# Optimization experiments

Measured on AMD Instinct MI355X. Metric: run time of the kernel, lower is better.

## Reference

```python
import jax, jax.numpy as jnp
import numpy as np

B, S, H = 1, 2048, 2048
NH, NKV, HD = 32, 8, 64
GROUPS = NH // NKV
KV_DIM = NKV * HD
COMP = int(S * 0.5)
FF = 5632  # round_up(2048*4*2/3, 256), fla GatedMLP convention
DEPTH = 2
EPS = 1e-6


def rmsnorm(x, w):
    var = jnp.mean(jnp.square(x), axis=-1, keepdims=True)
    return x * jax.lax.rsqrt(var + EPS) * w


def setup_inputs() -> dict:
    key = jax.random.key(0)
    ks = jax.random.split(key, 10)
    sc = 0.02
    return {
        "hidden_states": jax.random.normal(ks[0], (B, S, H), jnp.float32),
        "comp_w": jax.random.normal(ks[1], (COMP, S), jnp.float32) * sc,
        "comp_b": jnp.zeros((COMP,), jnp.float32),
        "q_w": jax.random.normal(ks[2], (H, H), jnp.float32) * sc,
        "k_w": jax.random.normal(ks[3], (KV_DIM, H), jnp.float32) * sc,
        "v_w": jax.random.normal(ks[4], (KV_DIM, H), jnp.float32) * sc,
        "o_w": jax.random.normal(ks[5], (H, H), jnp.float32) * sc,
        "attn_norm_w": jnp.ones((H,), jnp.float32),
        "mlp_norm_w": jnp.ones((H,), jnp.float32),
        "gate_w": jax.random.normal(ks[6], (FF, H), jnp.float32) * sc,
        "up_w": jax.random.normal(ks[7], (FF, H), jnp.float32) * sc,
        "down_w": jax.random.normal(ks[8], (H, FF), jnp.float32) * sc,
    }


def reference(hidden_states, comp_w, comp_b, q_w, k_w, v_w, o_w,
              attn_norm_w, mlp_norm_w, gate_w, up_w, down_w):
    # init_compressed_tokens: Linear over the sequence axis
    # (b,s,h) -> transpose -> (b,h,s) @ W^T -> (b,h,c) -> transpose -> (b,c,h)
    compressed = jnp.einsum('bsh,cs->bch', hidden_states, comp_w) + comp_b[None, :, None]

    for _ in range(DEPTH):
        residual = jnp.concatenate([hidden_states, compressed], axis=1)  # (b, s+c, h)
        ct = rmsnorm(compressed, attn_norm_w)
        q = (ct @ q_w.T).reshape(B, COMP, NH, HD)
        k = (residual @ k_w.T).reshape(B, S + COMP, NKV, HD)
        v = (residual @ v_w.T).reshape(B, S + COMP, NKV, HD)
        # GQA expand (repeat_interleave along head dim)
        k = jnp.repeat(k, GROUPS, axis=2)
        v = jnp.repeat(v, GROUPS, axis=2)
        scores = jnp.einsum('bsnk,btnk->bsnt', q, k) / (HD ** 0.5)
        attn = jax.nn.softmax(scores, axis=-1)
        o = jnp.einsum('bsnt,btnk->bsnk', attn, v).reshape(B, COMP, H)
        compressed = o @ o_w.T + ct
        ct2 = rmsnorm(compressed, mlp_norm_w)
        mlp_out = (jax.nn.silu(ct2 @ gate_w.T) * (ct2 @ up_w.T)) @ down_w.T
        compressed = mlp_out + ct2
    return compressed
```

## Files before the change

### kernel.cpp

```cpp
#include <hip/hip_runtime.h>
#include <math.h>

constexpr int S_   = 2048;
constexpr int H_   = 2048;
constexpr int NH_  = 32;
constexpr int NKV_ = 8;
constexpr int HD_  = 64;
constexpr int GROUPS_ = NH_ / NKV_;
constexpr int KV_  = NKV_ * HD_;
constexpr int KV2_ = 2 * KV_;
constexpr int COMP_ = 1024;
constexpr int FF_  = 5632;
constexpr int GU2_ = 2 * FF_;
constexpr int TOT_ = S_ + COMP_;
constexpr float EPS_ = 1e-6f;
constexpr int SK_ = 4;
constexpr int SP_ = 2;
constexpr float LOG2E_ = 1.44269504088896340736f;

typedef __attribute__((ext_vector_type(4))) float f32x4;
typedef __attribute__((ext_vector_type(8))) short bf16x8;
typedef __attribute__((ext_vector_type(8))) ushort u16x8;

__device__ __forceinline__ ushort f2bf(float x) {
    union { float f; unsigned u; } v; v.f = x;
    unsigned r = v.u + 0x7fffu + ((v.u >> 16) & 1u);
    return (ushort)(r >> 16);
}
__device__ __forceinline__ float bf2f(ushort x) {
    union { unsigned u; float f; } v; v.u = ((unsigned)x) << 16;
    return v.f;
}
__device__ __forceinline__ uint cvtpk_bf16(float lo, float hi) {
    uint r;
    asm("v_cvt_pk_bf16_f32 %0, %1, %2" : "=v"(r) : "v"(lo), "v"(hi));
    return r;
}

__global__ __launch_bounds__(256) void f2b_k(
    const float* __restrict__ x, ushort* __restrict__ y, int n4)
{
    int i = blockIdx.x * 256 + threadIdx.x;
    const int stride = gridDim.x * 256;
    for (; i < n4; i += stride) {
        float4 v = ((const float4*)x)[i];
        ushort4 r = {f2bf(v.x), f2bf(v.y), f2bf(v.z), f2bf(v.w)};
        ((ushort4*)y)[i] = r;
    }
}

__global__ __launch_bounds__(256) void f2b_gu(
    const float* __restrict__ gate, const float* __restrict__ up,
    ushort* __restrict__ dst, int n4)
{
    constexpr int H4 = H_ / 4;
    int i = blockIdx.x * 256 + threadIdx.x;
    const int stride = gridDim.x * 256;
    for (; i < n4; i += stride) {
        const int j = i / H4, c4 = i - j * H4;
        const float* src = ((j >> 4) & 1) ? up : gate;
        const int srow = ((j >> 5) << 4) | (j & 15);
        const float4 v = ((const float4*)src)[srow * H4 + c4];
        ushort4 r = {f2bf(v.x), f2bf(v.y), f2bf(v.z), f2bf(v.w)};
        ((ushort4*)dst)[i] = r;
    }
}

__global__ __launch_bounds__(256) void tpose64(
    const ushort* __restrict__ in, ushort* __restrict__ out,
    int R, int C, int ldi)
{
    __shared__ ushort T[64][72];
    const int r0 = blockIdx.x * 64, c0 = blockIdx.y * 64;
    const int row = threadIdx.x >> 2, seg = threadIdx.x & 3;

    const ushort* g = &in[(size_t)(r0 + row) * ldi + c0 + seg * 16];
    *(u16x8*)&T[row][seg * 16]     = *(const u16x8*)g;
    *(u16x8*)&T[row][seg * 16 + 8] = *(const u16x8*)(g + 8);
    __syncthreads();

    ushort tmp[16];
#pragma unroll
    for (int j = 0; j < 16; j++) tmp[j] = T[seg * 16 + j][row];
    ushort* go = &out[(size_t)(c0 + row) * R + r0 + seg * 16];
    *(u16x8*)go       = *(const u16x8*)&tmp[0];
    *(u16x8*)(go + 8) = *(const u16x8*)&tmp[8];
}

#define BARS do { __builtin_amdgcn_s_barrier(); __builtin_amdgcn_sched_barrier(0); } while (0)
#define VMW(n) asm volatile("s_waitcnt vmcnt(" #n ")" ::: "memory")
#define STG(gp, lp) __builtin_amdgcn_global_load_lds( \
    (const __attribute__((address_space(1))) void*)(gp), \
    (__attribute__((address_space(3))) void*)(lp), 16, 0, 0)
#define STA(bufA, R0, kt) STG(Ag + (size_t)(R0) * K + (kt) * 64, &(bufA)[((R0) + w * 8) * 64])
#define STB(bufB, R0, kt) STG(Bg + (size_t)(R0) * K + (kt) * 64, &(bufB)[((R0) + w * 8) * 64])

__device__ __forceinline__ void ldaq(bf16x8 (&aa)[2][2], const ushort* bufA,
                                     int m0, int aoff, int s0, int s1)
{
#pragma unroll
    for (int m = 0; m < 2; m++) {
        aa[m][0] = *(const bf16x8*)&bufA[aoff + (m0 + m) * 1024 + s0];
        aa[m][1] = *(const bf16x8*)&bufA[aoff + (m0 + m) * 1024 + s1];
    }
}
__device__ __forceinline__ void ldbq(bf16x8 (&bb)[4][2], const ushort* bufB,
                                     int boff, int s0, int s1)
{
#pragma unroll
    for (int nt = 0; nt < 4; nt++) {
        bb[nt][0] = *(const bf16x8*)&bufB[boff + nt * 1024 + s0];
        bb[nt][1] = *(const bf16x8*)&bufB[boff + nt * 1024 + s1];
    }
}
template <int M0>
__device__ __forceinline__ void mfmaq(f32x4 (&acc)[8][4], bf16x8 (&aa)[2][2],
                                      bf16x8 (&bb)[4][2])
{
    __builtin_amdgcn_s_setprio(1);
#pragma unroll
    for (int m = 0; m < 2; m++)
#pragma unroll
        for (int nt = 0; nt < 4; nt++) {
            acc[M0 + m][nt] = __builtin_amdgcn_mfma_f32_16x16x32_bf16(
                aa[m][0], bb[nt][0], acc[M0 + m][nt], 0, 0, 0);
            acc[M0 + m][nt] = __builtin_amdgcn_mfma_f32_16x16x32_bf16(
                aa[m][1], bb[nt][1], acc[M0 + m][nt], 0, 0, 0);
        }
    __builtin_amdgcn_s_setprio(0);
}

__global__ __launch_bounds__(512, 2) void gemm8ph(
    const ushort* __restrict__ A, const ushort* __restrict__ B,
    ushort* __restrict__ g, int N, int K)
{
    alignas(16) __shared__ ushort lds[4][16384];
    ushort* const lA0 = lds[0];
    ushort* const lB0 = lds[1];
    ushort* const lA1 = lds[2];
    ushort* const lB1 = lds[3];

    const int tid = threadIdx.x;
    const int w = tid >> 6, lane = tid & 63;
    const int wr = w >> 2, wc = w & 3;
    const int fr = lane & 15, fq = lane >> 4;
    const int xk = fr & 7;

    const int nwg = gridDim.x;
    const int nbn = N >> 8;
    int id = (int)blockIdx.x;
    if (!(nwg & 7)) id = (id & 7) * (nwg >> 3) + (id >> 3);
    const int bm = id / nbn, bn = id - bm * nbn;

    const int srow = lane >> 3;
    const int scol = ((lane & 7) ^ srow) << 3;
    const ushort* Ag = A + (size_t)(bm * 256 + w * 8 + srow) * K + scol;
    const ushort* Bg = B + (size_t)(bn * 256 + w * 8 + srow) * K + scol;

    const int aoff = (wr * 128 + fr) * 64;
    const int boff = (wc * 64 + fr) * 64;
    const int s0 = ((0 + fq) ^ xk) << 3;
    const int s1 = ((4 + fq) ^ xk) << 3;

    f32x4 acc[8][4];
#pragma unroll
    for (int i = 0; i < 8; i++)
#pragma unroll
        for (int j = 0; j < 4; j++) acc[i][j] = (f32x4){0.f, 0.f, 0.f, 0.f};

    bf16x8 aa[2][2], bb[4][2];

    STB(lB0, 0, 0);   STB(lB0, 64, 0);
    STA(lA0, 0, 0);   STA(lA0, 128, 0);
    STB(lB0, 128, 0); STB(lB0, 192, 0);
    STA(lA0, 64, 0);  STA(lA0, 192, 0);
    STB(lB1, 0, 1);   STB(lB1, 64, 1);
    STA(lA1, 0, 1);   STA(lA1, 128, 1);
    STB(lB1, 128, 1); STB(lB1, 192, 1);
    VMW(6);
    BARS;

    const int NITER = K >> 7;
    for (int i = 0; i < NITER - 1; i++) {
        const int t1 = 2 * i + 1, t2 = 2 * i + 2, t3 = 2 * i + 3;
        ldbq(bb, lB0, boff, s0, s1);
        ldaq(aa, lA0, 0, aoff, s0, s1);
        STA(lA1, 64, t1); STA(lA1, 192, t1);
        BARS; mfmaq<0>(acc, aa, bb); BARS;
        ldaq(aa, lA0, 2, aoff, s0, s1);
        STB(lB0, 0, t2); STB(lB0, 64, t2);
        BARS; mfmaq<2>(acc, aa, bb); BARS;
        ldaq(aa, lA0, 4, aoff, s0, s1);
        STA(lA0, 0, t2); STA(lA0, 128, t2);
        BARS; mfmaq<4>(acc, aa, bb); BARS;
        ldaq(aa, lA0, 6, aoff, s0, s1);
        STB(lB0, 128, t2); STB(lB0, 192, t2);
        BARS; mfmaq<6>(acc, aa, bb); VMW(6); BARS;
        ldbq(bb, lB1, boff, s0, s1);
        ldaq(aa, lA1, 0, aoff, s0, s1);
        STA(lA0, 64, t2); STA(lA0, 192, t2);
        BARS; mfmaq<0>(acc, aa, bb); BARS;
        ldaq(aa, lA1, 2, aoff, s0, s1);
        STB(lB1, 0, t3); STB(lB1, 64, t3);
        BARS; mfmaq<2>(acc, aa, bb); BARS;
        ldaq(aa, lA1, 4, aoff, s0, s1);
        STA(lA1, 0, t3); STA(lA1, 128, t3);
        BARS; mfmaq<4>(acc, aa, bb); BARS;
        ldaq(aa, lA1, 6, aoff, s0, s1);
        STB(lB1, 128, t3); STB(lB1, 192, t3);
        BARS; mfmaq<6>(acc, aa, bb); VMW(6); BARS;
    }
    {
        const int t1 = 2 * NITER - 1;
        ldbq(bb, lB0, boff, s0, s1);
        ldaq(aa, lA0, 0, aoff, s0, s1);
        STA(lA1, 64, t1); STA(lA1, 192, t1);
        BARS; mfmaq<0>(acc, aa, bb); BARS;
        ldaq(aa, lA0, 2, aoff, s0, s1);
        BARS; mfmaq<2>(acc, aa, bb); BARS;
        ldaq(aa, lA0, 4, aoff, s0, s1);
        BARS; mfmaq<4>(acc, aa, bb); BARS;
        ldaq(aa, lA0, 6, aoff, s0, s1);
        BARS; mfmaq<6>(acc, aa, bb); VMW(0); BARS;
        ldbq(bb, lB1, boff, s0, s1);
        ldaq(aa, lA1, 0, aoff, s0, s1);
        BARS; mfmaq<0>(acc, aa, bb); BARS;
        ldaq(aa, lA1, 2, aoff, s0, s1);
        BARS; mfmaq<2>(acc, aa, bb); BARS;
        ldaq(aa, lA1, 4, aoff, s0, s1);
        BARS; mfmaq<4>(acc, aa, bb); BARS;
        ldaq(aa, lA1, 6, aoff, s0, s1);
        mfmaq<6>(acc, aa, bb);
    }

    const int FFo = N >> 1;
#pragma unroll
    for (int mt = 0; mt < 8; mt++) {
#pragma unroll
        for (int u = 0; u < 2; u++) {
            const int col = (bn * 8 + wc * 2 + u) * 16 + fr;
#pragma unroll
            for (int r = 0; r < 4; r++) {
                const int row = bm * 256 + wr * 128 + mt * 16 + fq * 4 + r;
                const float xg = acc[mt][2 * u][r];
                const float xu = acc[mt][2 * u + 1][r];
                const float yv = xg / (1.f + __expf(-xg)) * xu;
                g[(size_t)row * FFo + col] = f2bf(yv);
            }
        }
    }
}

__global__ __launch_bounds__(256) void mfma_gemm_sk(
    const ushort* __restrict__ A, const ushort* __restrict__ B,
    float* __restrict__ part, int M, int N, int K, int Kc)
{
    __shared__ ushort Alds[128 * 32];
    __shared__ ushort Blds[128 * 32];

    const int tid  = threadIdx.x;
    const int w    = tid >> 6;
    const int lane = tid & 63;
    const int bm = blockIdx.y, bn = blockIdx.x, z = blockIdx.z;
    const int wr = w >> 1, wc = w & 1;
    const int fr = lane & 15;
    const int fq = lane >> 4;
    const int srow = lane >> 2;
    const int skof = (lane & 3) * 8;

    f32x4 acc[4][4];
#pragma unroll
    for (int i = 0; i < 4; i++)
#pragma unroll
        for (int j = 0; j < 4; j++)
            acc[i][j] = (f32x4){0.f, 0.f, 0.f, 0.f};

    const int kbeg = z * Kc;
    for (int k0 = kbeg; k0 < kbeg + Kc; k0 += 32) {
        __syncthreads();
#pragma unroll
        for (int i = 0; i < 2; i++) {
            const int slot = w * 2 + i;
            const ushort* ga = &A[(size_t)(bm * 128 + slot * 16 + srow) * K + k0 + skof];
            __builtin_amdgcn_global_load_lds(
                (const __attribute__((address_space(1))) void*)ga,
                (__attribute__((address_space(3))) void*)&Alds[slot * 512], 16, 0, 0);
            const ushort* gb = &B[(size_t)(bn * 128 + slot * 16 + srow) * K + k0 + skof];
            __builtin_amdgcn_global_load_lds(
                (const __attribute__((address_space(1))) void*)gb,
                (__attribute__((address_space(3))) void*)&Blds[slot * 512], 16, 0, 0);
        }
        __syncthreads();

        bf16x8 a[4], b[4];
#pragma unroll
        for (int mt = 0; mt < 4; mt++)
            a[mt] = *(const bf16x8*)&Alds[(wr * 64 + mt * 16 + fr) * 32 + fq * 8];
#pragma unroll
        for (int nt = 0; nt < 4; nt++)
            b[nt] = *(const bf16x8*)&Blds[(wc * 64 + nt * 16 + fr) * 32 + fq * 8];

#pragma unroll
        for (int mt = 0; mt < 4; mt++)
#pragma unroll
            for (int nt = 0; nt < 4; nt++)
                acc[mt][nt] = __builtin_amdgcn_mfma_f32_16x16x32_bf16(
                    a[mt], b[nt], acc[mt][nt], 0, 0, 0);
    }

    float* pz = part + (size_t)z * M * N;
#pragma unroll
    for (int mt = 0; mt < 4; mt++)
#pragma unroll
        for (int nt = 0; nt < 4; nt++)
#pragma unroll
            for (int r = 0; r < 4; r++) {
                const int row = bm * 128 + wr * 64 + mt * 16 + fq * 4 + r;
                const int col = bn * 128 + wc * 64 + nt * 16 + fr;
                pz[(size_t)row * N + col] = acc[mt][nt][r];
            }
}

__global__ __launch_bounds__(256) void sk_reduce(
    const float* __restrict__ part, int mn4, int n4,
    const float* __restrict__ bias, const float* __restrict__ addp,
    float oscale, float* __restrict__ outf, ushort* __restrict__ outb)
{
    const size_t mn = (size_t)mn4 * 4;
    int i = blockIdx.x * 256 + threadIdx.x;
    const int stride = gridDim.x * 256;
    for (; i < mn4; i += stride) {
        float4 v = ((const float4*)part)[i];
#pragma unroll
        for (int z = 1; z < SK_; z++) {
            const float4 pz = ((const float4*)(part + z * mn))[i];
            v.x += pz.x; v.y += pz.y; v.z += pz.z; v.w += pz.w;
        }
        v.x *= oscale; v.y *= oscale; v.z *= oscale; v.w *= oscale;
        if (bias) {
            const float bb = bias[i / n4];
            v.x += bb; v.y += bb; v.z += bb; v.w += bb;
        }
        if (addp) {
            const float4 ad = ((const float4*)addp)[i];
            v.x += ad.x; v.y += ad.y; v.z += ad.z; v.w += ad.w;
        }
        if (outf) ((float4*)outf)[i] = v;
        if (outb) {
            ushort4 r = {f2bf(v.x), f2bf(v.y), f2bf(v.z), f2bf(v.w)};
            ((ushort4*)outb)[i] = r;
        }
    }
}

__global__ __launch_bounds__(256) void sk_reduce_rms(
    const float* __restrict__ part, const float* __restrict__ bias,
    const float* __restrict__ addp, const float* __restrict__ w,
    ushort* __restrict__ residb, float* __restrict__ y,
    ushort* __restrict__ yb)
{
    constexpr size_t MN = (size_t)COMP_ * H_;
    const int row = blockIdx.x;
    const int t = threadIdx.x;
    __shared__ float red[256];

    float4 v[2];
#pragma unroll
    for (int j = 0; j < 2; j++) {
        const int c4 = t + j * 256;
        v[j] = ((const float4*)(part + (size_t)row * H_))[c4];
#pragma unroll
        for (int z = 1; z < SK_; z++) {
            const float4 pz = ((const float4*)(part + z * MN + (size_t)row * H_))[c4];
            v[j].x += pz.x; v[j].y += pz.y; v[j].z += pz.z; v[j].w += pz.w;
        }
        if (bias) {
            const float bb = bias[row];
            v[j].x += bb; v[j].y += bb; v[j].z += bb; v[j].w += bb;
        }
        if (addp) {
            const float4 ad = ((const float4*)(addp + (size_t)row * H_))[c4];
            v[j].x += ad.x; v[j].y += ad.y; v[j].z += ad.z; v[j].w += ad.w;
        }
        if (residb) {
            ushort4 r = {f2bf(v[j].x), f2bf(v[j].y), f2bf(v[j].z), f2bf(v[j].w)};
            ((ushort4*)(residb + (size_t)row * H_))[c4] = r;
        }
    }
    float s = 0.f;
#pragma unroll
    for (int j = 0; j < 2; j++)
        s += v[j].x * v[j].x + v[j].y * v[j].y + v[j].z * v[j].z + v[j].w * v[j].w;
    red[t] = s;
    __syncthreads();
    for (int k = 128; k > 0; k >>= 1) {
        if (t < k) red[t] += red[t + k];
        __syncthreads();
    }
    const float scale = rsqrtf(red[0] * (1.0f / H_) + EPS_);
#pragma unroll
    for (int j = 0; j < 2; j++) {
        const int c4 = t + j * 256;
        const float4 wv = ((const float4*)w)[c4];
        float4 nv;
        nv.x = v[j].x * scale * wv.x;
        nv.y = v[j].y * scale * wv.y;
        nv.z = v[j].z * scale * wv.z;
        nv.w = v[j].w * scale * wv.w;
        ((float4*)(y + (size_t)row * H_))[c4] = nv;
        ushort4 r = {f2bf(nv.x), f2bf(nv.y), f2bf(nv.z), f2bf(nv.w)};
        ((ushort4*)(yb + (size_t)row * H_))[c4] = r;
    }
}

__global__ __launch_bounds__(256) void attn_mfma(
    const ushort* __restrict__ q, const ushort* __restrict__ k, int ldk,
    const ushort* __restrict__ vt, float* __restrict__ attp,
    float* __restrict__ ml)
{
    constexpr int KSPAN = TOT_ / SP_;
    alignas(16) __shared__ ushort Kb[2][8 * 512];
    alignas(16) __shared__ ushort Vb[2][8 * 512];
    alignas(16) __shared__ ushort Ps[64 * 64];

    const int qt = blockIdx.x, h = blockIdx.y, z = blockIdx.z;
    const int kvh = h / GROUPS_;
    const int tid = threadIdx.x;
    const int w = tid >> 6, lane = tid & 63;
    const int fr = lane & 15, fq = lane >> 4;
    const int q0 = qt * 64;

    const ushort* qrow = &q[(size_t)(q0 + w * 16 + fr) * H_ + h * HD_];
    const bf16x8 bq0 = *(const bf16x8*)(qrow + fq * 8);
    const bf16x8 bq1 = *(const bf16x8*)(qrow + 32 + fq * 8);

    float m = -1e30f, l = 0.f;
    f32x4 acc[4];
#pragma unroll
    for (int nt = 0; nt < 4; nt++) acc[nt] = (f32x4){0.f, 0.f, 0.f, 0.f};

    const int t_beg = z * KSPAN;
    const ushort* kp = &k[(size_t)(t_beg + w * 16 + fr) * ldk + kvh * HD_ + fq * 8];
    const ushort* vp = &vt[(size_t)(kvh * HD_ + w * 16 + fr) * TOT_ + t_beg + fq * 8];

#define ASTG(gp, lp) __builtin_amdgcn_global_load_lds( \
    (const __attribute__((address_space(1))) void*)(gp), \
    (__attribute__((address_space(3))) void*)(lp), 16, 0, 0)

    ASTG(kp,      &Kb[0][w * 512]);
    ASTG(kp + 32, &Kb[0][(4 + w) * 512]);
    ASTG(vp,      &Vb[0][w * 512]);
    ASTG(vp + 32, &Vb[0][(4 + w) * 512]);
    asm volatile("s_waitcnt vmcnt(0)" ::: "memory");
    __syncthreads();
    const ushort* kn = kp + (size_t)64 * ldk;
    const ushort* vn = vp + 64;

    const int pxor = (fr & 7) << 4;
    char* const psb = (char*)&Ps[(w * 16 + fr) * 64];

    const int NT = KSPAN / 64;
    int cur = 0;
    for (int t = 0; t < NT; t++) {
        f32x4 st[4];
        __builtin_amdgcn_s_setprio(1);
#pragma unroll
        for (int nt = 0; nt < 4; nt++) {
            const bf16x8 a0 = *(const bf16x8*)&Kb[cur][(nt * 64 + lane) * 8];
            const bf16x8 a1 = *(const bf16x8*)&Kb[cur][((4 + nt) * 64 + lane) * 8];
            f32x4 tacc = (f32x4){0.f, 0.f, 0.f, 0.f};
            tacc = __builtin_amdgcn_mfma_f32_16x16x32_bf16(a0, bq0, tacc, 0, 0, 0);
            tacc = __builtin_amdgcn_mfma_f32_16x16x32_bf16(a1, bq1, tacc, 0, 0, 0);
            st[nt] = tacc;
        }
        __builtin_amdgcn_s_setprio(0);

        if (t + 1 < NT) {
            ASTG(kn,      &Kb[cur ^ 1][w * 512]);
            ASTG(kn + 32, &Kb[cur ^ 1][(4 + w) * 512]);
            ASTG(vn,      &Vb[cur ^ 1][w * 512]);
            ASTG(vn + 32, &Vb[cur ^ 1][(4 + w) * 512]);
            kn += (size_t)64 * ldk;
            vn += 64;
        }

        float mt = st[0][0];
#pragma unroll
        for (int nt = 0; nt < 4; nt++)
#pragma unroll
            for (int r = 0; r < 4; r++) mt = fmaxf(mt, st[nt][r]);
        mt = fmaxf(mt, __shfl_xor(mt, 16));
        mt = fmaxf(mt, __shfl_xor(mt, 32));
        if (!__all(mt <= m + 8.0f)) {
            const float mnew = fmaxf(m, mt);
            const float alpha = exp2f(m - mnew);
            m = mnew;
            l *= alpha;
            const float ar0 = __shfl(alpha, fq * 4 + 0, 16);
            const float ar1 = __shfl(alpha, fq * 4 + 1, 16);
            const float ar2 = __shfl(alpha, fq * 4 + 2, 16);
            const float ar3 = __shfl(alpha, fq * 4 + 3, 16);
#pragma unroll
            for (int nt = 0; nt < 4; nt++) {
                acc[nt][0] *= ar0; acc[nt][1] *= ar1;
                acc[nt][2] *= ar2; acc[nt][3] *= ar3;
            }
        }
        float ss = 0.f;
#pragma unroll
        for (int nt = 0; nt < 4; nt++)
#pragma unroll
            for (int r = 0; r < 4; r++) {
                const float pv = exp2f(st[nt][r] - m);
                st[nt][r] = pv;
                ss += pv;
            }
        ss += __shfl_xor(ss, 16);
        ss += __shfl_xor(ss, 32);
        l += ss;

#pragma unroll
        for (int nt = 0; nt < 4; nt++) {
            uint2 uu;
            uu.x = cvtpk_bf16(st[nt][0], st[nt][1]);
            uu.y = cvtpk_bf16(st[nt][2], st[nt][3]);
            *(uint2*)(psb + ((nt * 32 + fq * 8) ^ pxor)) = uu;
        }
        const bf16x8 ap0 = *(const bf16x8*)(psb + ((fq * 16) ^ pxor));
        const bf16x8 ap1 = *(const bf16x8*)(psb + ((64 + fq * 16) ^ pxor));

        __builtin_amdgcn_s_setprio(1);
#pragma unroll
        for (int nt = 0; nt < 4; nt++) {
            const bf16x8 b0 = *(const bf16x8*)&Vb[cur][(nt * 64 + lane) * 8];
            const bf16x8 b1 = *(const bf16x8*)&Vb[cur][((4 + nt) * 64 + lane) * 8];
            acc[nt] = __builtin_amdgcn_mfma_f32_16x16x32_bf16(ap0, b0, acc[nt], 0, 0, 0);
            acc[nt] = __builtin_amdgcn_mfma_f32_16x16x32_bf16(ap1, b1, acc[nt], 0, 0, 0);
        }
        __builtin_amdgcn_s_setprio(0);

        asm volatile("s_waitcnt vmcnt(0)" ::: "memory");
        __syncthreads();
        cur ^= 1;
    }
#undef ASTG

    float* pz = attp + (size_t)z * COMP_ * H_;
#pragma unroll
    for (int r = 0; r < 4; r++) {
        const int row = q0 + w * 16 + fq * 4 + r;
#pragma unroll
        for (int nt = 0; nt < 4; nt++)
            pz[(size_t)row * H_ + h * HD_ + nt * 16 + fr] = acc[nt][r];
    }
    if (lane < 16)
        ((float2*)ml)[((size_t)z * NH_ + h) * COMP_ + (q0 + w * 16 + fr)] =
            make_float2(m, l);
}

__global__ __launch_bounds__(256) void attn_merge(
    const float* __restrict__ attp, const float* __restrict__ ml,
    ushort* __restrict__ o, int n4)
{
    constexpr int H4 = H_ / 4;
    constexpr size_t PS = (size_t)COMP_ * H_;
    int i = blockIdx.x * 256 + threadIdx.x;
    const int stride = gridDim.x * 256;
    for (; i < n4; i += stride) {
        const int row = i / H4;
        const int col = (i - row * H4) * 4;
        const int h = col >> 6;
        const float2 ml0 = ((const float2*)ml)[((size_t)0 * NH_ + h) * COMP_ + row];
        const float2 ml1 = ((const float2*)ml)[((size_t)1 * NH_ + h) * COMP_ + row];
        const float M = fmaxf(ml0.x, ml1.x);
        const float a0 = exp2f(ml0.x - M), a1 = exp2f(ml1.x - M);
        const float inv = 1.0f / (a0 * ml0.y + a1 * ml1.y);
        const float4 p0 = ((const float4*)attp)[i];
        const float4 p1 = ((const float4*)(attp + PS))[i];
        ushort4 r = {f2bf((a0 * p0.x + a1 * p1.x) * inv),
                     f2bf((a0 * p0.y + a1 * p1.y) * inv),
                     f2bf((a0 * p0.z + a1 * p1.z) * inv),
                     f2bf((a0 * p0.w + a1 * p1.w) * inv)};
        ((ushort4*)o)[i] = r;
    }
}

extern "C" void kernel_launch(void* const* d_in, const int* in_sizes, int n_in,
                              void* d_out, int out_size, void* d_ws, size_t ws_size,
                              hipStream_t stream)
{
    (void)in_sizes; (void)n_in; (void)out_size; (void)ws_size;

    const float* hidden      = (const float*)d_in[0];
    const float* comp_w      = (const float*)d_in[1];
    const float* comp_b      = (const float*)d_in[2];
    const float* q_w         = (const float*)d_in[3];
    const float* k_w         = (const float*)d_in[4];
    const float* v_w         = (const float*)d_in[5];
    const float* o_w         = (const float*)d_in[6];
    const float* attn_norm_w = (const float*)d_in[7];
    const float* mlp_norm_w  = (const float*)d_in[8];
    const float* gate_w      = (const float*)d_in[9];
    const float* up_w        = (const float*)d_in[10];
    const float* down_w      = (const float*)d_in[11];
    float* out = (float*)d_out;

    char* p = (char*)d_ws;
    auto alloc = [&](size_t bytes) -> char* {
        char* r = p; p += (bytes + 255) & ~(size_t)255; return r;
    };
    ushort* qw_bf    = (ushort*)alloc((size_t)H_ * H_ * 2);
    ushort* kvw_bf   = (ushort*)alloc((size_t)KV2_ * H_ * 2);
    ushort* ow_bf    = (ushort*)alloc((size_t)H_ * H_ * 2);
    ushort* guw_bf   = (ushort*)alloc((size_t)GU2_ * H_ * 2);
    ushort* down_bf  = (ushort*)alloc((size_t)H_ * FF_ * 2);
    ushort* compw_bf = (ushort*)alloc((size_t)COMP_ * S_ * 2);
    ushort* hidcomp  = (ushort*)alloc((size_t)TOT_ * H_ * 2);
    ushort* hidT     = (ushort*)alloc((size_t)H_ * S_ * 2);
    ushort* ct_bf    = (ushort*)alloc((size_t)COMP_ * H_ * 2);
    ushort* ct2_bf   = (ushort*)alloc((size_t)COMP_ * H_ * 2);
    ushort* ob_bf    = (ushort*)alloc((size_t)COMP_ * H_ * 2);
    ushort* qb_bf    = (ushort*)alloc((size_t)COMP_ * H_ * 2);
    ushort* kvb_bf   = (ushort*)alloc((size_t)TOT_ * KV2_ * 2);
    ushort* vt_bf    = (ushort*)alloc((size_t)KV_ * TOT_ * 2);
    ushort* gb_bf    = (ushort*)alloc((size_t)COMP_ * FF_ * 2);
    float* ct    = (float*)alloc((size_t)COMP_ * H_ * 4);
    float* ct2   = (float*)alloc((size_t)COMP_ * H_ * 4);
    float*  skbuf = (float*)alloc((size_t)SK_ * TOT_ * KV2_ * 4);
    float*  attp  = skbuf;
    float*  mlbuf = skbuf + (size_t)SP_ * COMP_ * H_;

    ushort* cur_bf = hidcomp + (size_t)S_ * H_;

    const dim3 blk(256);

    f2b_k<<<512, blk, 0, stream>>>(q_w,    qw_bf,            H_ * H_ / 4);
    f2b_k<<<512, blk, 0, stream>>>(k_w,    kvw_bf,           KV_ * H_ / 4);
    f2b_k<<<512, blk, 0, stream>>>(v_w,    kvw_bf + (size_t)KV_ * H_, KV_ * H_ / 4);
    f2b_k<<<512, blk, 0, stream>>>(o_w,    ow_bf,            H_ * H_ / 4);
    f2b_gu<<<1024, blk, 0, stream>>>(gate_w, up_w, guw_bf,   GU2_ * H_ / 4);
    f2b_k<<<512, blk, 0, stream>>>(down_w, down_bf,          H_ * FF_ / 4);
    f2b_k<<<512, blk, 0, stream>>>(comp_w, compw_bf,         COMP_ * S_ / 4);
    f2b_k<<<512, blk, 0, stream>>>(hidden, hidcomp,          S_ * H_ / 4);
    tpose64<<<dim3(S_ / 64, H_ / 64), blk, 0, stream>>>(hidcomp, hidT, S_, H_, H_);

    mfma_gemm_sk<<<dim3(H_ / 128, COMP_ / 128, SK_), blk, 0, stream>>>(
        compw_bf, hidT, skbuf, COMP_, H_, S_, S_ / SK_);
    sk_reduce_rms<<<COMP_, blk, 0, stream>>>(
        skbuf, comp_b, nullptr, attn_norm_w, cur_bf, ct, ct_bf);

    for (int d = 0; d < 2; d++) {
        mfma_gemm_sk<<<dim3(H_ / 128, COMP_ / 128, SK_), blk, 0, stream>>>(
            ct_bf, qw_bf, skbuf, COMP_, H_, H_, H_ / SK_);
        sk_reduce<<<1024, blk, 0, stream>>>(
            skbuf, COMP_ * H_ / 4, H_ / 4, nullptr, nullptr, 0.125f * LOG2E_,
            nullptr, qb_bf);

        mfma_gemm_sk<<<dim3(KV2_ / 128, TOT_ / 128, SK_), blk, 0, stream>>>(
            hidcomp, kvw_bf, skbuf, TOT_, KV2_, H_, H_ / SK_);
        sk_reduce<<<1024, blk, 0, stream>>>(
            skbuf, TOT_ * KV2_ / 4, KV2_ / 4, nullptr, nullptr, 1.f, nullptr, kvb_bf);

        tpose64<<<dim3(TOT_ / 64, KV_ / 64), blk, 0, stream>>>(
            kvb_bf + KV_, vt_bf, TOT_, KV_, KV2_);

        attn_mfma<<<dim3(COMP_ / 64, NH_, SP_), blk, 0, stream>>>(
            qb_bf, kvb_bf, KV2_, vt_bf, attp, mlbuf);
        attn_merge<<<512, blk, 0, stream>>>(attp, mlbuf, ob_bf, COMP_ * H_ / 4);

        mfma_gemm_sk<<<dim3(H_ / 128, COMP_ / 128, SK_), blk, 0, stream>>>(
            ob_bf, ow_bf, skbuf, COMP_, H_, H_, H_ / SK_);
        sk_reduce_rms<<<COMP_, blk, 0, stream>>>(
            skbuf, nullptr, ct, mlp_norm_w, nullptr, ct2, ct2_bf);

        gemm8ph<<<dim3((GU2_ / 256) * (COMP_ / 256)), dim3(512), 0, stream>>>(
            ct2_bf, guw_bf, gb_bf, GU2_, H_);

        mfma_gemm_sk<<<dim3(H_ / 128, COMP_ / 128, SK_), blk, 0, stream>>>(
            gb_bf, down_bf, skbuf, COMP_, H_, FF_, FF_ / SK_);
        if (d == 0) {
            sk_reduce_rms<<<COMP_, blk, 0, stream>>>(
                skbuf, nullptr, ct2, attn_norm_w, cur_bf, ct, ct_bf);
        } else {
            sk_reduce<<<1024, blk, 0, stream>>>(
                skbuf, COMP_ * H_ / 4, H_ / 4, nullptr, ct2, 1.f, out, nullptr);
        }
    }
}
```

Before: 833.8 us.

## Fuse weight conversions into one launch and use MFMA-fragment LDS layout

Seven separate fp32-to-bf16 conversion launches are merged into a single grid-stride kernel that picks its source and destination by index range, which removes per-launch overhead and tail idle time. Separately, the split-K GEMM's global-to-LDS loads now assign lanes so that each 16-row slot is stored in exactly the order the MFMA fragment reads it. Each lane then reads its operand as one contiguous 16-byte chunk at lane*8, which is meant to avoid LDS bank conflicts on the fragment reads. The trade-off is that each lane's global load now strides across rows rather than along a row, which may coalesce less well.

Result: slower. 856.0 us (+2.7%).

```diff
diff --git a/kernel.cpp b/kernel.cpp
--- a/kernel.cpp
+++ b/kernel.cpp
@@ -37,15 +37,36 @@
     return r;
 }
 
-__global__ __launch_bounds__(256) void f2b_k(
-    const float* __restrict__ x, ushort* __restrict__ y, int n4)
-{
+__global__ __launch_bounds__(256) void f2b_all(
+    const float* __restrict__ s0, ushort* __restrict__ d0,
+    const float* __restrict__ s1, ushort* __restrict__ d1,
+    const float* __restrict__ s2, ushort* __restrict__ d2,
+    const float* __restrict__ s3, ushort* __restrict__ d3,
+    const float* __restrict__ s4, ushort* __restrict__ d4,
+    const float* __restrict__ s5, ushort* __restrict__ d5,
+    const float* __restrict__ s6, ushort* __restrict__ d6)
+{
+    constexpr int B0 = H_ * H_ / 4;
+    constexpr int B1 = B0 + KV_ * H_ / 4;
+    constexpr int B2 = B1 + KV_ * H_ / 4;
+    constexpr int B3 = B2 + H_ * H_ / 4;
+    constexpr int B4 = B3 + H_ * FF_ / 4;
+    constexpr int B5 = B4 + COMP_ * S_ / 4;
+    constexpr int B6 = B5 + S_ * H_ / 4;
     int i = blockIdx.x * 256 + threadIdx.x;
     const int stride = gridDim.x * 256;
-    for (; i < n4; i += stride) {
-        float4 v = ((const float4*)x)[i];
+    for (; i < B6; i += stride) {
+        const float* s; ushort* d; int off;
+        if      (i < B0) { s = s0; d = d0; off = i; }
+        else if (i < B1) { s = s1; d = d1; off = i - B0; }
+        else if (i < B2) { s = s2; d = d2; off = i - B1; }
+        else if (i < B3) { s = s3; d = d3; off = i - B2; }
+        else if (i < B4) { s = s4; d = d4; off = i - B3; }
+        else if (i < B5) { s = s5; d = d5; off = i - B4; }
+        else             { s = s6; d = d6; off = i - B5; }
+        const float4 v = ((const float4*)s)[off];
         ushort4 r = {f2bf(v.x), f2bf(v.y), f2bf(v.z), f2bf(v.w)};
-        ((ushort4*)y)[i] = r;
+        ((ushort4*)d)[off] = r;
     }
 }
 
@@ -265,8 +286,8 @@
     const int wr = w >> 1, wc = w & 1;
     const int fr = lane & 15;
     const int fq = lane >> 4;
-    const int srow = lane >> 2;
-    const int skof = (lane & 3) * 8;
+    const int srow = lane & 15;
+    const int skof = (lane >> 4) * 8;
 
     f32x4 acc[4][4];
 #pragma unroll
@@ -295,10 +316,10 @@
         bf16x8 a[4], b[4];
 #pragma unroll
         for (int mt = 0; mt < 4; mt++)
-            a[mt] = *(const bf16x8*)&Alds[(wr * 64 + mt * 16 + fr) * 32 + fq * 8];
+            a[mt] = *(const bf16x8*)&Alds[(wr * 4 + mt) * 512 + lane * 8];
 #pragma unroll
         for (int nt = 0; nt < 4; nt++)
-            b[nt] = *(const bf16x8*)&Blds[(wc * 64 + nt * 16 + fr) * 32 + fq * 8];
+            b[nt] = *(const bf16x8*)&Blds[(wc * 4 + nt) * 512 + lane * 8];
 
 #pragma unroll
         for (int mt = 0; mt < 4; mt++)
@@ -634,14 +655,15 @@
 
     const dim3 blk(256);
 
-    f2b_k<<<512, blk, 0, stream>>>(q_w,    qw_bf,            H_ * H_ / 4);
-    f2b_k<<<512, blk, 0, stream>>>(k_w,    kvw_bf,           KV_ * H_ / 4);
-    f2b_k<<<512, blk, 0, stream>>>(v_w,    kvw_bf + (size_t)KV_ * H_, KV_ * H_ / 4);
-    f2b_k<<<512, blk, 0, stream>>>(o_w,    ow_bf,            H_ * H_ / 4);
+    f2b_all<<<2048, blk, 0, stream>>>(
+        q_w, qw_bf,
+        k_w, kvw_bf,
+        v_w, kvw_bf + (size_t)KV_ * H_,
+        o_w, ow_bf,
+        down_w, down_bf,
+        comp_w, compw_bf,
+        hidden, hidcomp);
     f2b_gu<<<1024, blk, 0, stream>>>(gate_w, up_w, guw_bf,   GU2_ * H_ / 4);
-    f2b_k<<<512, blk, 0, stream>>>(down_w, down_bf,          H_ * FF_ / 4);
-    f2b_k<<<512, blk, 0, stream>>>(comp_w, compw_bf,         COMP_ * S_ / 4);
-    f2b_k<<<512, blk, 0, stream>>>(hidden, hidcomp,          S_ * H_ / 4);
     tpose64<<<dim3(S_ / 64, H_ / 64), blk, 0, stream>>>(hidcomp, hidT, S_, H_, H_);
 
     mfma_gemm_sk<<<dim3(H_ / 128, COMP_ / 128, SK_), blk, 0, stream>>>(
```
